# Kernel tuning notes

Measured on AMD Instinct MI355X. Metric: run time of the kernel, lower is better.

## Reference

```python
import jax, jax.numpy as jnp
import numpy as np

USER_NUM = 100000
ITEM_NUM = 50000
N_NODES = USER_NUM + ITEM_NUM
NNZ = 4800000
EMB = 64
N_LAYERS = 3
EPS = 0.2
NORM_EPS = 1e-12  # matches torch F.normalize eps clamp


def setup_inputs() -> dict:
    key = jax.random.key(0)
    ks = jax.random.split(key, 6)
    user_emb = jax.random.normal(ks[0], (USER_NUM, EMB), dtype=jnp.float32)
    item_emb = jax.random.normal(ks[1], (ITEM_NUM, EMB), dtype=jnp.float32)
    adj_rows = jax.random.randint(ks[2], (NNZ,), 0, N_NODES, dtype=jnp.int32)
    adj_cols = jax.random.randint(ks[3], (NNZ,), 0, N_NODES, dtype=jnp.int32)
    adj_vals = jax.random.uniform(ks[4], (NNZ,), dtype=jnp.float32)
    noise = jax.random.uniform(ks[5], (N_LAYERS, N_NODES, EMB), dtype=jnp.float32)
    return {"user_emb": user_emb, "item_emb": item_emb, "adj_rows": adj_rows,
            "adj_cols": adj_cols, "adj_vals": adj_vals, "noise": noise}


def reference(user_emb, item_emb, adj_rows, adj_cols, adj_vals, noise):
    # ego: [N, d]
    ego = jnp.concatenate([user_emb, item_emb], axis=0)

    def spmm(x):
        # sparse_norm_adj @ x via COO gather + segment-sum scatter
        return jax.ops.segment_sum(adj_vals[:, None] * x[adj_cols], adj_rows,
                                   num_segments=N_NODES)

    layer_outs = []
    for k in range(N_LAYERS):
        ego = spmm(ego)
        # perturbed=True branch: ego += sign(ego) * l2_normalize(noise) * eps
        r = noise[k]
        r_unit = r / jnp.maximum(jnp.linalg.norm(r, axis=-1, keepdims=True), NORM_EPS)
        ego = ego + jnp.sign(ego) * r_unit * EPS
        layer_outs.append(ego)

    all_emb = jnp.mean(jnp.stack(layer_outs, axis=1), axis=1)  # [N, d]
    return all_emb[:USER_NUM], all_emb[USER_NUM:]
```

## Files before the change

kernel.cpp:

```cpp
#include <hip/hip_runtime.h>

typedef unsigned int uint;

#define USER_NUM   100000
#define ITEM_NUM   50000
#define N_NODES    (USER_NUM + ITEM_NUM)
#define NNZ        4800000
#define EMB        64
#define EPS_F      0.2f
#define NORM_EPS_F 1e-12f

#define RB_SHIFT   8
#define RB         256
#define NB         ((N_NODES + RB - 1) / RB)
#define CAP        9216
#define BINA_CHUNK 8192
#define BINA_GRID  ((NNZ + BINA_CHUNK - 1) / BINA_CHUNK)

__device__ inline float bflo(uint u) { return __uint_as_float(u << 16); }
__device__ inline float bfhi(uint u) { return __uint_as_float(u & 0xffff0000u); }
__device__ inline uint f2bf(float f) {
    uint u = __float_as_uint(f);
    return (u + 0x7fffu + ((u >> 16) & 1u)) >> 16;
}
__device__ inline uint pack2(float a, float b) { return f2bf(a) | (f2bf(b) << 16); }


__global__ void init_gcursor(int* __restrict__ g) {
    int b = blockIdx.x * blockDim.x + threadIdx.x;
    if (b < NB) g[b] = b * CAP;
}

__global__ __launch_bounds__(1024) void binA_kernel(const int* __restrict__ rows,
                                                    const int* __restrict__ cols,
                                                    const float* __restrict__ vals,
                                                    int* __restrict__ gcursor,
                                                    int2* __restrict__ staging) {
    __shared__ int2 data[BINA_CHUNK];
    __shared__ unsigned short bid[BINA_CHUNK];
    __shared__ int hist[NB];
    __shared__ int rstart[NB + 1];
    __shared__ int gbase[NB];
    __shared__ int lcur[NB];
    __shared__ int wsum[16];
    int t = threadIdx.x;
    int cbeg = blockIdx.x * BINA_CHUNK;
    int cend = min(cbeg + BINA_CHUNK, NNZ);
    int total = cend - cbeg;

    int r[8];
    if (t < NB) hist[t] = 0;
    __syncthreads();
#pragma unroll
    for (int k = 0; k < 8; ++k) {
        int i = cbeg + (k << 10) + t;
        r[k] = (i < cend) ? rows[i] : -1;
        if (r[k] >= 0) atomicAdd(&hist[r[k] >> RB_SHIFT], 1);
    }
    __syncthreads();

    int v = (t < NB) ? hist[t] : 0;
    int sc = v;
#pragma unroll
    for (int off = 1; off < 64; off <<= 1) {
        int u = __shfl_up(sc, off, 64);
        if ((t & 63) >= off) sc += u;
    }
    if ((t & 63) == 63) wsum[t >> 6] = sc;
    __syncthreads();
    if (t < 64) {
        int ws = (t < 16) ? wsum[t] : 0;
#pragma unroll
        for (int off = 1; off < 16; off <<= 1) {
            int u = __shfl_up(ws, off, 64);
            if (t >= off) ws += u;
        }
        if (t < 16) wsum[t] = ws;
    }
    __syncthreads();
    int wid = t >> 6;
    int excl = sc - v + ((wid > 0) ? wsum[wid - 1] : 0);
    if (t <= NB) rstart[t] = excl;
    if (t < NB) {
        gbase[t] = atomicAdd(&gcursor[t], hist[t]);
        lcur[t] = 0;
    }
    __syncthreads();

#pragma unroll
    for (int k = 0; k < 8; ++k) {
        if (r[k] >= 0) {
            int i = cbeg + (k << 10) + t;
            int b = r[k] >> RB_SHIFT;
            int pos = rstart[b] + atomicAdd(&lcur[b], 1);
            data[pos] = make_int2(((r[k] & (RB - 1)) << 18) | cols[i],
                                  __float_as_int(vals[i]));
            bid[pos] = (unsigned short)b;
        }
    }
    __syncthreads();

    for (int i = t; i < total; i += 1024) {
        int b = bid[i];
        staging[(long)gbase[b] + (i - rstart[b])] = data[i];
    }
}

__global__ __launch_bounds__(1024) void bscan_kernel(const int* __restrict__ gcursor,
                                                     int* __restrict__ bucket_base,
                                                     int* __restrict__ row_ptr) {
    __shared__ int wsum[16];
    int t = threadIdx.x;
    int c = (t < NB) ? (gcursor[t] - t * CAP) : 0;
    int sc = c;
#pragma unroll
    for (int off = 1; off < 64; off <<= 1) {
        int u = __shfl_up(sc, off, 64);
        if ((t & 63) >= off) sc += u;
    }
    if ((t & 63) == 63) wsum[t >> 6] = sc;
    __syncthreads();
    if (t < 64) {
        int ws = (t < 16) ? wsum[t] : 0;
#pragma unroll
        for (int off = 1; off < 16; off <<= 1) {
            int u = __shfl_up(ws, off, 64);
            if (t >= off) ws += u;
        }
        if (t < 16) wsum[t] = ws;
    }
    __syncthreads();
    int wid = t >> 6;
    int excl = sc - c + ((wid > 0) ? wsum[wid - 1] : 0);
    if (t < NB) bucket_base[t] = excl;
    if (t == 0) row_ptr[N_NODES] = NNZ;
}

__global__ __launch_bounds__(512) void binB_kernel(const int* __restrict__ gcursor,
                                                   const int* __restrict__ bucket_base,
                                                   const int2* __restrict__ staging,
                                                   int2* __restrict__ edges,
                                                   int* __restrict__ row_ptr) {
    __shared__ int2 sorted[CAP];
    __shared__ int s[RB];
    __shared__ int cur[RB];
    __shared__ int wsum[8];
    int b = blockIdx.x;
    int t = threadIdx.x;
    int cnt = gcursor[b] - b * CAP;
    long sbase = (long)b * CAP;
    int base = bucket_base[b];

    if (t < RB) s[t] = 0;
    __syncthreads();
    for (int i = t; i < cnt; i += 512)
        atomicAdd(&s[((unsigned)staging[sbase + i].x) >> 18], 1);
    __syncthreads();

    int v = (t < RB) ? s[t] : 0;
    int sc = v;
#pragma unroll
    for (int off = 1; off < 64; off <<= 1) {
        int u = __shfl_up(sc, off, 64);
        if ((t & 63) >= off) sc += u;
    }
    if ((t & 63) == 63) wsum[t >> 6] = sc;
    __syncthreads();
    if (t < 64) {
        int ws = (t < 8) ? wsum[t] : 0;
#pragma unroll
        for (int off = 1; off < 8; off <<= 1) {
            int u = __shfl_up(ws, off, 64);
            if (t >= off) ws += u;
        }
        if (t < 8) wsum[t] = ws;
    }
    __syncthreads();
    int wid = t >> 6;
    int excl = sc - v + ((wid > 0) ? wsum[wid - 1] : 0);

    int row = (b << RB_SHIFT) + t;
    if (t < RB) {
        if (row < N_NODES) row_ptr[row] = base + excl;
        cur[t] = excl;
    }
    __syncthreads();
    for (int i = t; i < cnt; i += 512) {
        int2 e = staging[sbase + i];
        int rl = ((unsigned)e.x) >> 18;
        int pos = atomicAdd(&cur[rl], 1);
        sorted[pos] = make_int2(e.x & ((1 << 18) - 1), e.y);
    }
    __syncthreads();
    for (int i = t; i < cnt; i += 512)
        edges[base + i] = sorted[i];
}

__global__ void convert_kernel(const float4* __restrict__ u, const float4* __restrict__ it,
                               uint2* __restrict__ xh) {
    const int NU4 = USER_NUM * EMB / 4;
    const int NT4 = N_NODES * EMB / 4;
    int i = blockIdx.x * blockDim.x + threadIdx.x;
    int stride = gridDim.x * blockDim.x;
    for (; i < NT4; i += stride) {
        float4 f = (i < NU4) ? u[i] : it[i - NU4];
        xh[i] = make_uint2(pack2(f.x, f.y), pack2(f.z, f.w));
    }
}

__global__ __launch_bounds__(256) void spmm_layer_kernel(const uint* __restrict__ x,
                                                         uint* __restrict__ x_out,
                                                         const int* __restrict__ row_ptr,
                                                         const int2* __restrict__ edges,
                                                         const float* __restrict__ noise_k,
                                                         float* __restrict__ out, int mode) {
    int lane = threadIdx.x & 63;
    int row = blockIdx.x * 4 + (threadIdx.x >> 6);
    if (row >= N_NODES) return;
    int g = lane >> 3;
    int sub = lane & 7;

    int beg = row_ptr[row];
    int end = row_ptr[row + 1];
    int lim = end - 1;

    float a0 = 0.f, a1 = 0.f, a2 = 0.f, a3 = 0.f;
    float a4 = 0.f, a5 = 0.f, a6 = 0.f, a7 = 0.f;

    for (int base = beg; base < end; base += 16) {
        int i0 = base + g, i1 = base + 8 + g;
        int2 e0 = edges[min(i0, lim)];
        int2 e1 = edges[min(i1, lim)];
        const uint4* q0 = (const uint4*)(x + (long)e0.x * (EMB / 2));
        const uint4* q1 = (const uint4*)(x + (long)e1.x * (EMB / 2));
        uint4 h0 = q0[sub];
        uint4 h1 = q1[sub];
        float w0 = (i0 < end) ? __int_as_float(e0.y) : 0.f;
        float w1 = (i1 < end) ? __int_as_float(e1.y) : 0.f;
        a0 += w0 * bflo(h0.x); a1 += w0 * bfhi(h0.x);
        a2 += w0 * bflo(h0.y); a3 += w0 * bfhi(h0.y);
        a4 += w0 * bflo(h0.z); a5 += w0 * bfhi(h0.z);
        a6 += w0 * bflo(h0.w); a7 += w0 * bfhi(h0.w);
        a0 += w1 * bflo(h1.x); a1 += w1 * bfhi(h1.x);
        a2 += w1 * bflo(h1.y); a3 += w1 * bfhi(h1.y);
        a4 += w1 * bflo(h1.z); a5 += w1 * bfhi(h1.z);
        a6 += w1 * bflo(h1.w); a7 += w1 * bfhi(h1.w);
    }

#pragma unroll
    for (int off = 8; off <= 32; off <<= 1) {
        a0 += __shfl_xor(a0, off, 64); a1 += __shfl_xor(a1, off, 64);
        a2 += __shfl_xor(a2, off, 64); a3 += __shfl_xor(a3, off, 64);
        a4 += __shfl_xor(a4, off, 64); a5 += __shfl_xor(a5, off, 64);
        a6 += __shfl_xor(a6, off, 64); a7 += __shfl_xor(a7, off, 64);
    }

    const float4* nz = (const float4*)(noise_k + (long)row * EMB);
    float4 n0 = nz[sub * 2];
    float4 n1 = nz[sub * 2 + 1];
    float ss = n0.x * n0.x + n0.y * n0.y + n0.z * n0.z + n0.w * n0.w
             + n1.x * n1.x + n1.y * n1.y + n1.z * n1.z + n1.w * n1.w;
    ss += __shfl_xor(ss, 1, 64);
    ss += __shfl_xor(ss, 2, 64);
    ss += __shfl_xor(ss, 4, 64);
    float s = EPS_F / fmaxf(sqrtf(ss), NORM_EPS_F);

    float v0 = a0 + ((a0 > 0.f) ? 1.f : ((a0 < 0.f) ? -1.f : 0.f)) * n0.x * s;
    float v1 = a1 + ((a1 > 0.f) ? 1.f : ((a1 < 0.f) ? -1.f : 0.f)) * n0.y * s;
    float v2 = a2 + ((a2 > 0.f) ? 1.f : ((a2 < 0.f) ? -1.f : 0.f)) * n0.z * s;
    float v3 = a3 + ((a3 > 0.f) ? 1.f : ((a3 < 0.f) ? -1.f : 0.f)) * n0.w * s;
    float v4 = a4 + ((a4 > 0.f) ? 1.f : ((a4 < 0.f) ? -1.f : 0.f)) * n1.x * s;
    float v5 = a5 + ((a5 > 0.f) ? 1.f : ((a5 < 0.f) ? -1.f : 0.f)) * n1.y * s;
    float v6 = a6 + ((a6 > 0.f) ? 1.f : ((a6 < 0.f) ? -1.f : 0.f)) * n1.z * s;
    float v7 = a7 + ((a7 > 0.f) ? 1.f : ((a7 < 0.f) ? -1.f : 0.f)) * n1.w * s;

    if (g == 0) {
        float4* po = (float4*)(out + (long)row * EMB);
        float4 f01 = make_float4(v0, v1, v2, v3);
        float4 f23 = make_float4(v4, v5, v6, v7);
        if (mode == 0) {
            po[sub * 2] = f01;
            po[sub * 2 + 1] = f23;
        } else if (mode == 1) {
            float4 o0 = po[sub * 2], o1 = po[sub * 2 + 1];
            o0.x += v0; o0.y += v1; o0.z += v2; o0.w += v3;
            o1.x += v4; o1.y += v5; o1.z += v6; o1.w += v7;
            po[sub * 2] = o0;
            po[sub * 2 + 1] = o1;
        } else {
            float4 o0 = po[sub * 2], o1 = po[sub * 2 + 1];
            o0.x = (o0.x + v0) * (1.f / 3.f); o0.y = (o0.y + v1) * (1.f / 3.f);
            o0.z = (o0.z + v2) * (1.f / 3.f); o0.w = (o0.w + v3) * (1.f / 3.f);
            o1.x = (o1.x + v4) * (1.f / 3.f); o1.y = (o1.y + v5) * (1.f / 3.f);
            o1.z = (o1.z + v6) * (1.f / 3.f); o1.w = (o1.w + v7) * (1.f / 3.f);
            po[sub * 2] = o0;
            po[sub * 2 + 1] = o1;
        }
        if (mode != 2) {
            uint4* ph = (uint4*)(x_out + (long)row * (EMB / 2));
            ph[sub] = make_uint4(pack2(v0, v1), pack2(v2, v3),
                                 pack2(v4, v5), pack2(v6, v7));
        }
    }
}


extern "C" void kernel_launch(void* const* d_in, const int* in_sizes, int n_in,
                              void* d_out, int out_size, void* d_ws, size_t ws_size,
                              hipStream_t stream) {
    const float* user_emb = (const float*)d_in[0];
    const float* item_emb = (const float*)d_in[1];
    const int*   adj_rows = (const int*)d_in[2];
    const int*   adj_cols = (const int*)d_in[3];
    const float* adj_vals = (const float*)d_in[4];
    const float* noise    = (const float*)d_in[5];
    float* out = (float*)d_out;

    char* ws = (char*)d_ws;
    size_t off = 0;
    auto alloc = [&](size_t bytes) {
        char* p = ws + off;
        off += (bytes + 15) & ~size_t(15);
        return p;
    };
    int*   row_ptr     = (int*)alloc((N_NODES + 1) * sizeof(int));
    int*   gcursor     = (int*)alloc(NB * sizeof(int));
    int*   bucket_base = (int*)alloc(NB * sizeof(int));
    int2*  edges       = (int2*)alloc((size_t)NNZ * sizeof(int2));
    int2*  staging     = (int2*)alloc((size_t)NB * CAP * sizeof(int2));
    uint* xh_a = (uint*)staging;
    uint* xh_b = (uint*)((char*)staging + (size_t)N_NODES * EMB * 2);

    init_gcursor<<<3, 256, 0, stream>>>(gcursor);
    binA_kernel<<<BINA_GRID, 1024, 0, stream>>>(adj_rows, adj_cols, adj_vals,
                                                gcursor, staging);
    bscan_kernel<<<1, 1024, 0, stream>>>(gcursor, bucket_base, row_ptr);
    binB_kernel<<<NB, 512, 0, stream>>>(gcursor, bucket_base, staging, edges, row_ptr);

    convert_kernel<<<2048, 256, 0, stream>>>((const float4*)user_emb,
                                             (const float4*)item_emb, (uint2*)xh_a);

    const int LGRID = (N_NODES + 3) / 4;
    const size_t NE = (size_t)N_NODES * EMB;
    spmm_layer_kernel<<<LGRID, 256, 0, stream>>>(xh_a, xh_b, row_ptr, edges,
                                                 noise + 0 * NE, out, 0);
    spmm_layer_kernel<<<LGRID, 256, 0, stream>>>(xh_b, xh_a, row_ptr, edges,
                                                 noise + 1 * NE, out, 1);
    spmm_layer_kernel<<<LGRID, 256, 0, stream>>>(xh_a, nullptr, row_ptr, edges,
                                                 noise + 2 * NE, out, 2);
}
```

Measured before the change: 743.8 us.

## Sort edges by column chunk within rows and process SpMM column-chunk-major per wave

binB now sorts each row's edges by a finer key (row plus column chunk of 32K nodes), so edges inside a row are grouped by source-column range. The SpMM kernel gives each wave 19 consecutive rows and accumulates them in LDS. It sweeps the five column chunks in the outer loop so the gathered embedding working set at any moment stays within one chunk, aiming for better L2 reuse of the gathered rows. The cost is an extra ballot/popcount pass over edges per row, LDS accumulation traffic, a much smaller grid of persistent-style blocks with possible load imbalance, and narrower scalar stores in the epilogue.

```diff
diff --git a/kernel.cpp b/kernel.cpp
--- a/kernel.cpp
+++ b/kernel.cpp
@@ -1,6 +1,7 @@
 #include <hip/hip_runtime.h>
 
 typedef unsigned int uint;
+typedef unsigned long long ull;
 
 #define USER_NUM   100000
 #define ITEM_NUM   50000
@@ -16,6 +17,12 @@
 #define CAP        9216
 #define BINA_CHUNK 8192
 #define BINA_GRID  ((NNZ + BINA_CHUNK - 1) / BINA_CHUNK)
+
+#define CSHIFT     15
+#define NCHUNK     5
+#define NKEY       2048
+#define RPW        19
+#define SPMM_BLOCKS 2048
 
 __device__ inline float bflo(uint u) { return __uint_as_float(u << 16); }
 __device__ inline float bfhi(uint u) { return __uint_as_float(u & 0xffff0000u); }
@@ -136,29 +143,31 @@
     if (t == 0) row_ptr[N_NODES] = NNZ;
 }
 
-__global__ __launch_bounds__(512) void binB_kernel(const int* __restrict__ gcursor,
-                                                   const int* __restrict__ bucket_base,
-                                                   const int2* __restrict__ staging,
-                                                   int2* __restrict__ edges,
-                                                   int* __restrict__ row_ptr) {
+__global__ __launch_bounds__(1024) void binB_kernel(const int* __restrict__ gcursor,
+                                                    const int* __restrict__ bucket_base,
+                                                    const int2* __restrict__ staging,
+                                                    int2* __restrict__ edges,
+                                                    int* __restrict__ row_ptr) {
     __shared__ int2 sorted[CAP];
-    __shared__ int s[RB];
-    __shared__ int cur[RB];
-    __shared__ int wsum[8];
+    __shared__ int s[NKEY];
+    __shared__ int cur[NKEY];
+    __shared__ int wsum[16];
     int b = blockIdx.x;
     int t = threadIdx.x;
     int cnt = gcursor[b] - b * CAP;
     long sbase = (long)b * CAP;
     int base = bucket_base[b];
 
-    if (t < RB) s[t] = 0;
-    __syncthreads();
-    for (int i = t; i < cnt; i += 512)
-        atomicAdd(&s[((unsigned)staging[sbase + i].x) >> 18], 1);
-    __syncthreads();
-
-    int v = (t < RB) ? s[t] : 0;
-    int sc = v;
+    s[t] = 0;
+    s[t + 1024] = 0;
+    __syncthreads();
+    for (int i = t; i < cnt; i += 1024)
+        atomicAdd(&s[((unsigned)staging[sbase + i].x) >> 15], 1);
+    __syncthreads();
+
+    int v0 = s[2 * t], v1 = s[2 * t + 1];
+    int pv = v0 + v1;
+    int sc = pv;
 #pragma unroll
     for (int off = 1; off < 64; off <<= 1) {
         int u = __shfl_up(sc, off, 64);
@@ -167,32 +176,34 @@
     if ((t & 63) == 63) wsum[t >> 6] = sc;
     __syncthreads();
     if (t < 64) {
-        int ws = (t < 8) ? wsum[t] : 0;
-#pragma unroll
-        for (int off = 1; off < 8; off <<= 1) {
+        int ws = (t < 16) ? wsum[t] : 0;
+#pragma unroll
+        for (int off = 1; off < 16; off <<= 1) {
             int u = __shfl_up(ws, off, 64);
             if (t >= off) ws += u;
         }
-        if (t < 8) wsum[t] = ws;
+        if (t < 16) wsum[t] = ws;
     }
     __syncthreads();
     int wid = t >> 6;
-    int excl = sc - v + ((wid > 0) ? wsum[wid - 1] : 0);
-
-    int row = (b << RB_SHIFT) + t;
+    int ex = sc - pv + ((wid > 0) ? wsum[wid - 1] : 0);
+    cur[2 * t] = ex;
+    cur[2 * t + 1] = ex + v0;
+    __syncthreads();
+
     if (t < RB) {
-        if (row < N_NODES) row_ptr[row] = base + excl;
-        cur[t] = excl;
-    }
-    __syncthreads();
-    for (int i = t; i < cnt; i += 512) {
+        int row = (b << RB_SHIFT) + t;
+        if (row < N_NODES) row_ptr[row] = base + cur[t << 3];
+    }
+    __syncthreads();
+    for (int i = t; i < cnt; i += 1024) {
         int2 e = staging[sbase + i];
-        int rl = ((unsigned)e.x) >> 18;
-        int pos = atomicAdd(&cur[rl], 1);
+        int key = ((unsigned)e.x) >> 15;
+        int pos = atomicAdd(&cur[key], 1);
         sorted[pos] = make_int2(e.x & ((1 << 18) - 1), e.y);
     }
     __syncthreads();
-    for (int i = t; i < cnt; i += 512)
+    for (int i = t; i < cnt; i += 1024)
         edges[base + i] = sorted[i];
 }
 
@@ -208,98 +219,127 @@
     }
 }
 
-__global__ __launch_bounds__(256) void spmm_layer_kernel(const uint* __restrict__ x,
-                                                         uint* __restrict__ x_out,
-                                                         const int* __restrict__ row_ptr,
-                                                         const int2* __restrict__ edges,
-                                                         const float* __restrict__ noise_k,
-                                                         float* __restrict__ out, int mode) {
+__global__ __launch_bounds__(256, 8) void spmm_layer_kernel(const uint* __restrict__ x,
+                                                            uint* __restrict__ x_out,
+                                                            const int* __restrict__ row_ptr,
+                                                            const int2* __restrict__ edges,
+                                                            const float* __restrict__ noise_k,
+                                                            float* __restrict__ out, int mode) {
+    __shared__ float accs[4][RPW * 64];
+    __shared__ unsigned short st[4][RPW][6];
     int lane = threadIdx.x & 63;
-    int row = blockIdx.x * 4 + (threadIdx.x >> 6);
-    if (row >= N_NODES) return;
+    int wv = threadIdx.x >> 6;
+    int wid = blockIdx.x * 4 + wv;
+    int r0 = wid * RPW;
+    if (r0 >= N_NODES) return;
+    int nr = min(RPW, N_NODES - r0);
     int g = lane >> 3;
     int sub = lane & 7;
 
-    int beg = row_ptr[row];
-    int end = row_ptr[row + 1];
-    int lim = end - 1;
-
-    float a0 = 0.f, a1 = 0.f, a2 = 0.f, a3 = 0.f;
-    float a4 = 0.f, a5 = 0.f, a6 = 0.f, a7 = 0.f;
-
-    for (int base = beg; base < end; base += 16) {
-        int i0 = base + g, i1 = base + 8 + g;
-        int2 e0 = edges[min(i0, lim)];
-        int2 e1 = edges[min(i1, lim)];
-        const uint4* q0 = (const uint4*)(x + (long)e0.x * (EMB / 2));
-        const uint4* q1 = (const uint4*)(x + (long)e1.x * (EMB / 2));
-        uint4 h0 = q0[sub];
-        uint4 h1 = q1[sub];
-        float w0 = (i0 < end) ? __int_as_float(e0.y) : 0.f;
-        float w1 = (i1 < end) ? __int_as_float(e1.y) : 0.f;
-        a0 += w0 * bflo(h0.x); a1 += w0 * bfhi(h0.x);
-        a2 += w0 * bflo(h0.y); a3 += w0 * bfhi(h0.y);
-        a4 += w0 * bflo(h0.z); a5 += w0 * bfhi(h0.z);
-        a6 += w0 * bflo(h0.w); a7 += w0 * bfhi(h0.w);
-        a0 += w1 * bflo(h1.x); a1 += w1 * bfhi(h1.x);
-        a2 += w1 * bflo(h1.y); a3 += w1 * bfhi(h1.y);
-        a4 += w1 * bflo(h1.z); a5 += w1 * bfhi(h1.z);
-        a6 += w1 * bflo(h1.w); a7 += w1 * bfhi(h1.w);
-    }
-
-#pragma unroll
-    for (int off = 8; off <= 32; off <<= 1) {
-        a0 += __shfl_xor(a0, off, 64); a1 += __shfl_xor(a1, off, 64);
-        a2 += __shfl_xor(a2, off, 64); a3 += __shfl_xor(a3, off, 64);
-        a4 += __shfl_xor(a4, off, 64); a5 += __shfl_xor(a5, off, 64);
-        a6 += __shfl_xor(a6, off, 64); a7 += __shfl_xor(a7, off, 64);
-    }
-
-    const float4* nz = (const float4*)(noise_k + (long)row * EMB);
-    float4 n0 = nz[sub * 2];
-    float4 n1 = nz[sub * 2 + 1];
-    float ss = n0.x * n0.x + n0.y * n0.y + n0.z * n0.z + n0.w * n0.w
-             + n1.x * n1.x + n1.y * n1.y + n1.z * n1.z + n1.w * n1.w;
-    ss += __shfl_xor(ss, 1, 64);
-    ss += __shfl_xor(ss, 2, 64);
-    ss += __shfl_xor(ss, 4, 64);
-    float s = EPS_F / fmaxf(sqrtf(ss), NORM_EPS_F);
-
-    float v0 = a0 + ((a0 > 0.f) ? 1.f : ((a0 < 0.f) ? -1.f : 0.f)) * n0.x * s;
-    float v1 = a1 + ((a1 > 0.f) ? 1.f : ((a1 < 0.f) ? -1.f : 0.f)) * n0.y * s;
-    float v2 = a2 + ((a2 > 0.f) ? 1.f : ((a2 < 0.f) ? -1.f : 0.f)) * n0.z * s;
-    float v3 = a3 + ((a3 > 0.f) ? 1.f : ((a3 < 0.f) ? -1.f : 0.f)) * n0.w * s;
-    float v4 = a4 + ((a4 > 0.f) ? 1.f : ((a4 < 0.f) ? -1.f : 0.f)) * n1.x * s;
-    float v5 = a5 + ((a5 > 0.f) ? 1.f : ((a5 < 0.f) ? -1.f : 0.f)) * n1.y * s;
-    float v6 = a6 + ((a6 > 0.f) ? 1.f : ((a6 < 0.f) ? -1.f : 0.f)) * n1.z * s;
-    float v7 = a7 + ((a7 > 0.f) ? 1.f : ((a7 < 0.f) ? -1.f : 0.f)) * n1.w * s;
-
-    if (g == 0) {
-        float4* po = (float4*)(out + (long)row * EMB);
-        float4 f01 = make_float4(v0, v1, v2, v3);
-        float4 f23 = make_float4(v4, v5, v6, v7);
-        if (mode == 0) {
-            po[sub * 2] = f01;
-            po[sub * 2 + 1] = f23;
-        } else if (mode == 1) {
-            float4 o0 = po[sub * 2], o1 = po[sub * 2 + 1];
-            o0.x += v0; o0.y += v1; o0.z += v2; o0.w += v3;
-            o1.x += v4; o1.y += v5; o1.z += v6; o1.w += v7;
-            po[sub * 2] = o0;
-            po[sub * 2 + 1] = o1;
-        } else {
-            float4 o0 = po[sub * 2], o1 = po[sub * 2 + 1];
-            o0.x = (o0.x + v0) * (1.f / 3.f); o0.y = (o0.y + v1) * (1.f / 3.f);
-            o0.z = (o0.z + v2) * (1.f / 3.f); o0.w = (o0.w + v3) * (1.f / 3.f);
-            o1.x = (o1.x + v4) * (1.f / 3.f); o1.y = (o1.y + v5) * (1.f / 3.f);
-            o1.z = (o1.z + v6) * (1.f / 3.f); o1.w = (o1.w + v7) * (1.f / 3.f);
-            po[sub * 2] = o0;
-            po[sub * 2 + 1] = o1;
-        }
+    float* ac = accs[wv];
+    for (int k = lane; k < RPW * 64; k += 64) ac[k] = 0.f;
+
+    for (int j = 0; j < nr; ++j) {
+        int r = r0 + j;
+        int beg = row_ptr[r], endd = row_ptr[r + 1];
+        int deg = endd - beg;
+        int c1 = 0, c2 = 0, c3 = 0, c4 = 0;
+        if (deg > 0 && deg <= 64) {
+            int2 e = edges[beg + min(lane, deg - 1)];
+            int ch = e.x >> CSHIFT;
+            bool val = lane < deg;
+            c1 = __popcll(__ballot(val && ch < 1));
+            c2 = __popcll(__ballot(val && ch < 2));
+            c3 = __popcll(__ballot(val && ch < 3));
+            c4 = __popcll(__ballot(val && ch < 4));
+        } else if (deg > 64) {
+            for (int w = beg; w < endd; w += 64) {
+                int rem = endd - w;
+                int2 e = edges[w + min(lane, rem - 1)];
+                int ch = e.x >> CSHIFT;
+                bool val = lane < rem;
+                c1 += __popcll(__ballot(val && ch < 1));
+                c2 += __popcll(__ballot(val && ch < 2));
+                c3 += __popcll(__ballot(val && ch < 3));
+                c4 += __popcll(__ballot(val && ch < 4));
+            }
+        }
+        if (lane == 0) {
+            st[wv][j][0] = 0;
+            st[wv][j][1] = (unsigned short)c1;
+            st[wv][j][2] = (unsigned short)c2;
+            st[wv][j][3] = (unsigned short)c3;
+            st[wv][j][4] = (unsigned short)c4;
+            st[wv][j][5] = (unsigned short)deg;
+        }
+    }
+
+    for (int c = 0; c < NCHUNK; ++c) {
+        for (int j = 0; j < nr; ++j) {
+            int lo16 = st[wv][j][c], hi16 = st[wv][j][c + 1];
+            if (lo16 >= hi16) continue;
+            int r = r0 + j;
+            int beg = row_ptr[r];
+            int lo = beg + lo16, hi = beg + hi16, lim = hi - 1;
+
+            float a0 = 0.f, a1 = 0.f, a2 = 0.f, a3 = 0.f;
+            float a4 = 0.f, a5 = 0.f, a6 = 0.f, a7 = 0.f;
+            for (int bb = lo; bb < hi; bb += 16) {
+                int i0 = bb + g, i1 = bb + 8 + g;
+                int2 e0 = edges[min(i0, lim)];
+                int2 e1 = edges[min(i1, lim)];
+                const uint4* q0 = (const uint4*)(x + (ull)(uint)e0.x * (EMB / 2));
+                const uint4* q1 = (const uint4*)(x + (ull)(uint)e1.x * (EMB / 2));
+                uint4 h0 = q0[sub];
+                uint4 h1 = q1[sub];
+                float w0 = (i0 < hi) ? __int_as_float(e0.y) : 0.f;
+                float w1 = (i1 < hi) ? __int_as_float(e1.y) : 0.f;
+                a0 += w0 * bflo(h0.x); a1 += w0 * bfhi(h0.x);
+                a2 += w0 * bflo(h0.y); a3 += w0 * bfhi(h0.y);
+                a4 += w0 * bflo(h0.z); a5 += w0 * bfhi(h0.z);
+                a6 += w0 * bflo(h0.w); a7 += w0 * bfhi(h0.w);
+                a0 += w1 * bflo(h1.x); a1 += w1 * bfhi(h1.x);
+                a2 += w1 * bflo(h1.y); a3 += w1 * bfhi(h1.y);
+                a4 += w1 * bflo(h1.z); a5 += w1 * bfhi(h1.z);
+                a6 += w1 * bflo(h1.w); a7 += w1 * bfhi(h1.w);
+            }
+#pragma unroll
+            for (int off = 8; off <= 32; off <<= 1) {
+                a0 += __shfl_xor(a0, off, 64); a1 += __shfl_xor(a1, off, 64);
+                a2 += __shfl_xor(a2, off, 64); a3 += __shfl_xor(a3, off, 64);
+                a4 += __shfl_xor(a4, off, 64); a5 += __shfl_xor(a5, off, 64);
+                a6 += __shfl_xor(a6, off, 64); a7 += __shfl_xor(a7, off, 64);
+            }
+            if (g == 0) {
+                float* ap = ac + j * 64 + sub * 8;
+                ap[0] += a0; ap[1] += a1; ap[2] += a2; ap[3] += a3;
+                ap[4] += a4; ap[5] += a5; ap[6] += a6; ap[7] += a7;
+            }
+        }
+    }
+
+    for (int j = 0; j < nr; ++j) {
+        int r = r0 + j;
+        float a = ac[j * 64 + lane];
+        float nv = noise_k[(ull)r * EMB + lane];
+        float ss = nv * nv;
+        ss += __shfl_xor(ss, 1, 64);
+        ss += __shfl_xor(ss, 2, 64);
+        ss += __shfl_xor(ss, 4, 64);
+        ss += __shfl_xor(ss, 8, 64);
+        ss += __shfl_xor(ss, 16, 64);
+        ss += __shfl_xor(ss, 32, 64);
+        float s = EPS_F / fmaxf(sqrtf(ss), NORM_EPS_F);
+        float sg = (a > 0.f) ? 1.f : ((a < 0.f) ? -1.f : 0.f);
+        float v = a + sg * nv * s;
+        ull o = (ull)r * EMB + lane;
+        if (mode == 0) out[o] = v;
+        else if (mode == 1) out[o] += v;
+        else out[o] = (out[o] + v) * (1.f / 3.f);
         if (mode != 2) {
-            uint4* ph = (uint4*)(x_out + (long)row * (EMB / 2));
-            ph[sub] = make_uint4(pack2(v0, v1), pack2(v2, v3),
-                                 pack2(v4, v5), pack2(v6, v7));
+            float v2 = __shfl_xor(v, 1, 64);
+            if (!(lane & 1))
+                x_out[(ull)r * (EMB / 2) + (lane >> 1)] = pack2(v, v2);
         }
     }
 }
@@ -335,17 +375,16 @@
     binA_kernel<<<BINA_GRID, 1024, 0, stream>>>(adj_rows, adj_cols, adj_vals,
                                                 gcursor, staging);
     bscan_kernel<<<1, 1024, 0, stream>>>(gcursor, bucket_base, row_ptr);
-    binB_kernel<<<NB, 512, 0, stream>>>(gcursor, bucket_base, staging, edges, row_ptr);
+    binB_kernel<<<NB, 1024, 0, stream>>>(gcursor, bucket_base, staging, edges, row_ptr);
 
     convert_kernel<<<2048, 256, 0, stream>>>((const float4*)user_emb,
                                              (const float4*)item_emb, (uint2*)xh_a);
 
-    const int LGRID = (N_NODES + 3) / 4;
     const size_t NE = (size_t)N_NODES * EMB;
-    spmm_layer_kernel<<<LGRID, 256, 0, stream>>>(xh_a, xh_b, row_ptr, edges,
-                                                 noise + 0 * NE, out, 0);
-    spmm_layer_kernel<<<LGRID, 256, 0, stream>>>(xh_b, xh_a, row_ptr, edges,
-                                                 noise + 1 * NE, out, 1);
-    spmm_layer_kernel<<<LGRID, 256, 0, stream>>>(xh_a, nullptr, row_ptr, edges,
-                                                 noise + 2 * NE, out, 2);
-}
+    spmm_layer_kernel<<<SPMM_BLOCKS, 256, 0, stream>>>(xh_a, xh_b, row_ptr, edges,
+                                                       noise + 0 * NE, out, 0);
+    spmm_layer_kernel<<<SPMM_BLOCKS, 256, 0, stream>>>(xh_b, xh_a, row_ptr, edges,
+                                                       noise + 1 * NE, out, 1);
+    spmm_layer_kernel<<<SPMM_BLOCKS, 256, 0, stream>>>(xh_a, nullptr, row_ptr, edges,
+                                                       noise + 2 * NE, out, 2);
+}
```

After: 1.245 ms. +67.4%, slower.
